# Kernel tuning notes

Hardware: AMD Instinct MI355X
Metric: run time of the kernel (lower is better)

## Reference

```python
import jax, jax.numpy as jnp
import numpy as np

EMBED = 768
HEADS = 12
HEAD_DIM = EMBED // HEADS
STREAMS = 4
SK_ITERS = 20
MLP_HIDDEN = 3072
EPS_SK = 1e-8
EPS_LN = 1e-5


def setup_inputs() -> dict:
    key = jax.random.key(0)
    ks = jax.random.split(key, 16)
    w = lambda k, shape: (jax.random.normal(k, shape, dtype=jnp.float32) * 0.02)
    return {
        "x": jax.random.normal(ks[0], (8, 1024, EMBED), dtype=jnp.float32),
        "ln1_g": jnp.ones((EMBED,), jnp.float32),
        "ln1_b": jnp.zeros((EMBED,), jnp.float32),
        "ln2_g": jnp.ones((EMBED,), jnp.float32),
        "ln2_b": jnp.zeros((EMBED,), jnp.float32),
        "qkv_w": w(ks[1], (3 * EMBED, EMBED)),
        "qkv_b": jnp.zeros((3 * EMBED,), jnp.float32),
        "proj_w": w(ks[2], (EMBED, EMBED)),
        "proj_b": jnp.zeros((EMBED,), jnp.float32),
        "fc1_w": w(ks[3], (MLP_HIDDEN, EMBED)),
        "fc1_b": jnp.zeros((MLP_HIDDEN,), jnp.float32),
        "fc2_w": w(ks[4], (EMBED, MLP_HIDDEN)),
        "fc2_b": jnp.zeros((EMBED,), jnp.float32),
        "a_hres": w(ks[5], (STREAMS, STREAMS)),
        "a_hpre": w(ks[6], (STREAMS,)),
        "a_hpost": w(ks[7], (STREAMS,)),
        "m_hres": w(ks[8], (STREAMS, STREAMS)),
        "m_hpre": w(ks[9], (STREAMS,)),
        "m_hpost": w(ks[10], (STREAMS,)),
    }


def layernorm(x, g, b):
    mu = x.mean(-1, keepdims=True)
    var = ((x - mu) ** 2).mean(-1, keepdims=True)
    return (x - mu) * jax.lax.rsqrt(var + EPS_LN) * g + b


def sinkhorn_knopp(logits):
    # logits: (n, n) -> doubly-stochastic (n, n); batch expansion in torch is redundant
    A = jnp.exp(logits)
    for _ in range(SK_ITERS):
        A = A / (A.sum(-1, keepdims=True) + EPS_SK)
        A = A / (A.sum(-2, keepdims=True) + EPS_SK)
    return A


def attention(x, qkv_w, qkv_b, proj_w, proj_b):
    B, N, D = x.shape
    qkv = x @ qkv_w.T + qkv_b                      # (B, N, 3D)
    qkv = qkv.reshape(B, N, 3, HEADS, HEAD_DIM)
    q, k, v = jnp.moveaxis(qkv, 2, 0)              # each (B, N, H, hd)
    scale = HEAD_DIM ** -0.5
    scores = jnp.einsum('bqhd,bkhd->bhqk', q, k) * scale
    attn = jax.nn.softmax(scores, axis=-1)
    out = jnp.einsum('bhqk,bkhd->bqhd', attn, v).reshape(B, N, D)
    return out @ proj_w.T + proj_b


def mlp(x, fc1_w, fc1_b, fc2_w, fc2_b):
    h = jax.nn.gelu(x @ fc1_w.T + fc1_b, approximate=False)
    return h @ fc2_w.T + fc2_b


def mhc(x, hres_logits, hpre_logits, hpost_logits, transform_fn):
    B, L, D = x.shape
    n, c = STREAMS, D // STREAMS
    xs = x.reshape(B, L, n, c)
    H_res = sinkhorn_knopp(hres_logits)            # (n, n)
    H_pre = jax.nn.softmax(hpre_logits)            # (n,)
    H_post = jax.nn.softmax(hpost_logits)          # (n,)
    x_pre = jnp.einsum('n,blnc->blc', H_pre, xs)   # weighted sum over streams
    x_pre_full = jnp.tile(x_pre, (1, 1, n))        # (B, L, D)
    t = transform_fn(x_pre_full)
    t_mean = t.reshape(B, L, n, c).mean(axis=2)    # (B, L, c)
    out = (jnp.einsum('nm,blmc->blnc', H_res, xs)
           + H_post[None, None, :, None] * t_mean[:, :, None, :])
    return out.reshape(B, L, D)


def reference(x, ln1_g, ln1_b, ln2_g, ln2_b, qkv_w, qkv_b, proj_w, proj_b,
              fc1_w, fc1_b, fc2_w, fc2_b,
              a_hres, a_hpre, a_hpost, m_hres, m_hpre, m_hpost):
    x = mhc(x, a_hres, a_hpre, a_hpost,
            lambda h: attention(layernorm(h, ln1_g, ln1_b), qkv_w, qkv_b, proj_w, proj_b))
    x = mhc(x, m_hres, m_hpre, m_hpost,
            lambda h: mlp(layernorm(h, ln2_g, ln2_b), fc1_w, fc1_b, fc2_w, fc2_b))
    return x
```

## Files before the change

kernel.cpp:

```cpp
#include <hip/hip_runtime.h>
#include <hip/hip_bf16.h>
#include <cstdint>
#include <cstddef>

#define EMBED 768
#define STREAMS 4
#define CHUNK 192
#define HEADS 12
#define HD 64
#define SEQ 1024
#define BATCH 8
#define TOKENS (BATCH * SEQ)
#define MLPH 3072

typedef __bf16 bf16;
typedef __bf16 bf16x4 __attribute__((ext_vector_type(4)));
typedef __bf16 bf16x8 __attribute__((ext_vector_type(8)));
typedef float f32x4 __attribute__((ext_vector_type(4)));
typedef float f32x16 __attribute__((ext_vector_type(16)));

#define GLDS16(gp, lp)                                                        \
  __builtin_amdgcn_global_load_lds(                                           \
      (const __attribute__((address_space(1))) void*)(gp),                    \
      (__attribute__((address_space(3))) void*)(lp), 16, 0, 0)

#define BARRIER() do { asm volatile("" ::: "memory");                         \
  __builtin_amdgcn_s_barrier(); asm volatile("" ::: "memory"); } while (0)

__global__ void hprep_kernel(const float* ar, const float* ap, const float* ao,
                             const float* mr, const float* mp, const float* mo,
                             float* HS) {
  if (threadIdx.x != 0) return;
  const float* L[2] = {ar, mr};
  const float* P[2] = {ap, mp};
  const float* O[2] = {ao, mo};
  for (int s = 0; s < 2; ++s) {
    float A[16];
    for (int i = 0; i < 16; ++i) A[i] = expf(L[s][i]);
    for (int it = 0; it < 20; ++it) {
      for (int r = 0; r < 4; ++r) {
        float rs = A[4*r] + A[4*r+1] + A[4*r+2] + A[4*r+3] + 1e-8f;
        for (int c = 0; c < 4; ++c) A[4*r+c] /= rs;
      }
      for (int c = 0; c < 4; ++c) {
        float cs = A[c] + A[4+c] + A[8+c] + A[12+c] + 1e-8f;
        for (int r = 0; r < 4; ++r) A[4*r+c] /= cs;
      }
    }
    float* dst = HS + s * 24;
    for (int i = 0; i < 16; ++i) dst[i] = A[i];
    {
      float m = fmaxf(fmaxf(P[s][0], P[s][1]), fmaxf(P[s][2], P[s][3]));
      float e[4], t = 0.f;
      for (int i = 0; i < 4; ++i) { e[i] = expf(P[s][i] - m); t += e[i]; }
      for (int i = 0; i < 4; ++i) dst[16 + i] = e[i] / t;
    }
    {
      float m = fmaxf(fmaxf(O[s][0], O[s][1]), fmaxf(O[s][2], O[s][3]));
      float e[4], t = 0.f;
      for (int i = 0; i < 4; ++i) { e[i] = expf(O[s][i] - m); t += e[i]; }
      for (int i = 0; i < 4; ++i) dst[20 + i] = e[i] / t;
    }
  }
}

__global__ void cvt_kernel(const float* __restrict__ in, bf16* __restrict__ out, int n4) {
  int i = blockIdx.x * 256 + threadIdx.x;
  const int st = gridDim.x * 256;
  for (; i < n4; i += st) {
    const float4 v = ((const float4*)in)[i];
    bf16x4 o = {(bf16)v.x, (bf16)v.y, (bf16)v.z, (bf16)v.w};
    *(bf16x4*)(out + (size_t)i * 4) = o;
  }
}

__global__ __launch_bounds__(256) void preln_kernel(
    const float* __restrict__ x, const float* __restrict__ H,
    const float* __restrict__ g, const float* __restrict__ b,
    bf16* __restrict__ out) {
  const int t = blockIdx.x;
  const float* xr = x + (size_t)t * EMBED;
  __shared__ float s[CHUNK];
  __shared__ float part[8];
  __shared__ float red[2];
  const int tid = threadIdx.x;
  float sv = 0.f;
  if (tid < CHUNK) {
    sv = H[0]*xr[tid] + H[1]*xr[CHUNK+tid] + H[2]*xr[2*CHUNK+tid] + H[3]*xr[3*CHUNK+tid];
    s[tid] = sv;
  }
  float sum = sv, sq = sv * sv;
  #pragma unroll
  for (int m = 32; m > 0; m >>= 1) {
    sum += __shfl_down(sum, m);
    sq  += __shfl_down(sq, m);
  }
  if ((tid & 63) == 0) { part[tid >> 6] = sum; part[4 + (tid >> 6)] = sq; }
  __syncthreads();
  if (tid == 0) {
    float S = part[0] + part[1] + part[2] + part[3];
    float Q = part[4] + part[5] + part[6] + part[7];
    float mu = S * (1.f / CHUNK);
    float var = Q * (1.f / CHUNK) - mu * mu;
    red[0] = mu;
    red[1] = rsqrtf(var + 1e-5f);
  }
  __syncthreads();
  const float mu = red[0], rs = red[1];
  bf16* orow = out + (size_t)t * EMBED;
  #pragma unroll
  for (int r = 0; r < 3; ++r) {
    const int d = tid + r * 256;
    const float v = (s[d % CHUNK] - mu) * rs * g[d] + b[d];
    orow[d] = (bf16)v;
  }
}

template <int GELU, int OUTF32>
__global__ __launch_bounds__(256) void gemm_bt(
    const bf16* __restrict__ A, const bf16* __restrict__ B,
    const float* __restrict__ bias, void* __restrict__ Cout,
    int M, int N, int K) {
  constexpr int BM = 128, BN = 128, BK = 32;
  __shared__ bf16 sA[3][BM * BK];
  __shared__ bf16 sB[3][BN * BK];
  const int tid  = threadIdx.x;
  const int lane = tid & 63;
  const int nwg = gridDim.x * gridDim.y;
  int Lw = blockIdx.y * gridDim.x + blockIdx.x;
  Lw = (Lw & 7) * (nwg >> 3) + (Lw >> 3);
  const int bm = (Lw / gridDim.x) * BM;
  const int bn = (Lw % gridDim.x) * BN;
  const int wave = tid >> 6;
  const int wr = (wave >> 1) * 64;
  const int wc = (wave & 1) * 64;
  f32x16 acc[2][2] = {};
  const int tr = tid >> 2;
  const int gt = tid & 3;
  const int gsw = (gt ^ ((tr >> 1) & 3)) * 8;
  const bf16* Ag = A + (size_t)(bm + tr) * K + gsw;
  const bf16* Bg = B + (size_t)(bn + tr) * K + gsw;
  const int lofs = tr * BK + gt * 8;
  const int r31 = lane & 31, rh = lane >> 5;
  const int asw = (r31 >> 1) & 3;
  const int nst = K / BK;
#define STAGE(buf, t)                                                         \
  do { const int bk_ = (t) * BK;                                              \
    GLDS16(Ag + bk_, sA[buf] + lofs);                                         \
    GLDS16(Ag + (size_t)64 * K + bk_, sA[buf] + lofs + 64 * BK);              \
    GLDS16(Bg + bk_, sB[buf] + lofs);                                         \
    GLDS16(Bg + (size_t)64 * K + bk_, sB[buf] + lofs + 64 * BK);              \
  } while (0)
  STAGE(0, 0);
  STAGE(1, 1);
  int cur = 0;
  for (int t = 0; t < nst; ++t) {
    if (t + 2 < nst) {
      const int nb = cur + 2 >= 3 ? cur - 1 : cur + 2;
      STAGE(nb, t + 2);
      asm volatile("s_waitcnt vmcnt(8)" ::: "memory");
    } else if (t + 1 < nst) {
      asm volatile("s_waitcnt vmcnt(4)" ::: "memory");
    } else {
      asm volatile("s_waitcnt vmcnt(0)" ::: "memory");
    }
    BARRIER();
    bf16x8 af[2][2], bfr[2][2];
    #pragma unroll
    for (int i = 0; i < 2; ++i)
      #pragma unroll
      for (int ks = 0; ks < 2; ++ks) {
        const int pos = ((ks * 2 + rh) ^ asw) * 8;
        af[i][ks]  = *(const bf16x8*)(sA[cur] + (wr + i * 32 + r31) * BK + pos);
        bfr[i][ks] = *(const bf16x8*)(sB[cur] + (wc + i * 32 + r31) * BK + pos);
      }
    #pragma unroll
    for (int ks = 0; ks < 2; ++ks)
      #pragma unroll
      for (int i = 0; i < 2; ++i)
        #pragma unroll
        for (int j = 0; j < 2; ++j)
          acc[i][j] = __builtin_amdgcn_mfma_f32_32x32x16_bf16(af[i][ks], bfr[j][ks], acc[i][j], 0, 0, 0);
    BARRIER();
    cur = cur == 2 ? 0 : cur + 1;
  }
#undef STAGE
  #pragma unroll
  for (int j = 0; j < 2; ++j) {
    const int col = bn + wc + j * 32 + r31;
    const float bv = bias[col];
    #pragma unroll
    for (int i = 0; i < 2; ++i) {
      const int row0 = bm + wr + i * 32 + 4 * rh;
      #pragma unroll
      for (int reg = 0; reg < 16; ++reg) {
        const int row = row0 + (reg & 3) + 8 * (reg >> 2);
        float v = acc[i][j][reg] + bv;
        if (GELU) v = 0.5f * v * (1.f + erff(v * 0.70710678118654752f));
        const size_t off = (size_t)row * N + col;
        if (OUTF32) ((float*)Cout)[off] = v;
        else        ((bf16*)Cout)[off] = (bf16)v;
      }
    }
  }
}

__global__ __launch_bounds__(256) void vt_kernel(const bf16* __restrict__ qkv,
                                                 bf16* __restrict__ VT) {
  const int tt = blockIdx.x;
  const int bh = blockIdx.y;
  const int bb = bh / HEADS;
  const int h = bh - bb * HEADS;
  __shared__ bf16 sT[64 * 64];
  const int t = threadIdx.x;
  const int srow = t >> 3;
  const int g = t & 7;
  const int gs = ((g ^ (srow & 7)) * 8);
  const bf16* Vg = qkv + ((size_t)(bb * SEQ + tt * 64 + srow)) * 2304 + 1536 + h * 64;
  GLDS16(Vg + gs, sT + srow * 64 + g * 8);
  GLDS16(Vg + (size_t)32 * 2304 + gs, sT + (32 + srow) * 64 + g * 8);
  __syncthreads();
  const int hd = t >> 2;
  const int tg = (t & 3) * 16;
  bf16 tmp[16];
  #pragma unroll
  for (int j = 0; j < 16; ++j) {
    const int tok = tg + j;
    tmp[j] = sT[tok * 64 + (hd ^ ((tok & 7) << 3))];
  }
  bf16* op = VT + (size_t)bh * (HD * SEQ) + (size_t)hd * SEQ + tt * 64 + tg;
  *(bf16x8*)(op) = *(const bf16x8*)(tmp);
  *(bf16x8*)(op + 8) = *(const bf16x8*)(tmp + 8);
}

__global__ __launch_bounds__(256) void attn_kernel(
    const bf16* __restrict__ qkv, const bf16* __restrict__ VT,
    bf16* __restrict__ out) {
  const int lin = blockIdx.x;
  const int qt = (lin >> 3) & 15;
  const int bh = (lin & 7) + 8 * (lin >> 7);
  const int bb = bh / HEADS;
  const int h = bh - bb * HEADS;
  const int tid = threadIdx.x;
  const int lane = tid & 63;
  const int wave = tid >> 6;
  const size_t tokBase = (size_t)bb * SEQ;
  const int q0 = qt * 64;

  __shared__ bf16 sQ[64 * 64];
  __shared__ bf16 sK[2][64 * 64];
  __shared__ bf16 sV[2][80 * 64];
  __shared__ bf16 sP[4][16 * 64];

  for (int idx = tid; idx < 16 * 64; idx += 256) {
    const bf16 v = (idx < 64) ? (bf16)1.f : (bf16)0.f;
    sV[0][64 * 64 + idx] = v;
    sV[1][64 * 64 + idx] = v;
  }

  const int srow = tid >> 3;
  const int g = tid & 7;
  const int gs = ((g ^ (srow & 7)) * 8);
  {
    const bf16* Qg = qkv + (tokBase + q0 + srow) * 2304 + h * 64;
    GLDS16(Qg + gs, sQ + srow * 64 + g * 8);
    GLDS16(Qg + (size_t)32 * 2304 + gs, sQ + (32 + srow) * 64 + g * 8);
  }
  __syncthreads();
  const int l15 = lane & 15, hi = lane >> 4;
  const int ksw = (l15 & 7) << 3;
  bf16x8 qf[2];
  {
    const int qrow = wave * 16 + l15;
    const int qsw = (qrow & 7) << 3;
    #pragma unroll
    for (int ks = 0; ks < 2; ++ks)
      qf[ks] = *(const bf16x8*)(sQ + qrow * 64 + ((hi * 8 + ks * 32) ^ qsw));
  }

  f32x4 o[5] = {};
  float mrun[4];
  #pragma unroll
  for (int r = 0; r < 4; ++r) mrun[r] = -1e30f;

  const bf16* Kbase = qkv + tokBase * 2304 + 768 + h * 64;
  const bf16* Vbase = VT + (size_t)bh * (HD * SEQ);

  {
    const bf16* Kg = Kbase + (size_t)srow * 2304;
    GLDS16(Kg + gs, sK[0] + srow * 64 + g * 8);
    GLDS16(Kg + (size_t)32 * 2304 + gs, sK[0] + (32 + srow) * 64 + g * 8);
    const bf16* Vg = Vbase + (size_t)srow * SEQ;
    GLDS16(Vg + gs, sV[0] + srow * 64 + g * 8);
    GLDS16(Vg + (size_t)32 * SEQ + gs, sV[0] + (32 + srow) * 64 + g * 8);
  }

  for (int it = 0; it < SEQ / 64; ++it) {
    const int cur = it & 1;
    if (it + 1 < SEQ / 64) {
      const int kb = (it + 1) * 64;
      const bf16* Kg = Kbase + (size_t)(kb + srow) * 2304;
      GLDS16(Kg + gs, sK[cur ^ 1] + srow * 64 + g * 8);
      GLDS16(Kg + (size_t)32 * 2304 + gs, sK[cur ^ 1] + (32 + srow) * 64 + g * 8);
      const bf16* Vg = Vbase + (size_t)srow * SEQ + kb;
      GLDS16(Vg + gs, sV[cur ^ 1] + srow * 64 + g * 8);
      GLDS16(Vg + (size_t)32 * SEQ + gs, sV[cur ^ 1] + (32 + srow) * 64 + g * 8);
      asm volatile("s_waitcnt vmcnt(4)" ::: "memory");
    } else {
      asm volatile("s_waitcnt vmcnt(0)" ::: "memory");
    }
    BARRIER();
    f32x4 s[4];
    #pragma unroll
    for (int nj = 0; nj < 4; ++nj) {
      s[nj] = (f32x4){0.f, 0.f, 0.f, 0.f};
      #pragma unroll
      for (int ks = 0; ks < 2; ++ks) {
        bf16x8 kf = *(const bf16x8*)(sK[cur] + (nj * 16 + l15) * 64 + ((hi * 8 + ks * 32) ^ ksw));
        s[nj] = __builtin_amdgcn_mfma_f32_16x16x32_bf16(qf[ks], kf, s[nj], 0, 0, 0);
      }
    }
    float tmax[4];
    #pragma unroll
    for (int r = 0; r < 4; ++r) {
      float m = fmaxf(fmaxf(s[0][r], s[1][r]), fmaxf(s[2][r], s[3][r]));
      tmax[r] = m * 0.125f;
    }
    #pragma unroll
    for (int r = 0; r < 4; ++r) {
      #pragma unroll
      for (int mm = 1; mm < 16; mm <<= 1) tmax[r] = fmaxf(tmax[r], __shfl_xor(tmax[r], mm));
    }
    bool need = false;
    #pragma unroll
    for (int r = 0; r < 4; ++r) need |= (tmax[r] > mrun[r]);
    if (__any(need)) {
      float alpha[4];
      #pragma unroll
      for (int r = 0; r < 4; ++r) {
        const float mnew = fmaxf(mrun[r], tmax[r]);
        alpha[r] = __expf(mrun[r] - mnew);
        mrun[r] = mnew;
      }
      #pragma unroll
      for (int nj = 0; nj < 5; ++nj)
        #pragma unroll
        for (int r = 0; r < 4; ++r)
          o[nj][r] *= alpha[r];
    }
    float p[4][4];
    #pragma unroll
    for (int r = 0; r < 4; ++r)
      #pragma unroll
      for (int nj = 0; nj < 4; ++nj)
        p[nj][r] = __expf(s[nj][r] * 0.125f - mrun[r]);
    bf16* Pw = sP[wave];
    #pragma unroll
    for (int r = 0; r < 4; ++r) {
      const int prow = hi * 4 + r;
      const int psw = (prow & 7) << 3;
      #pragma unroll
      for (int nj = 0; nj < 4; ++nj)
        Pw[prow * 64 + ((nj * 16 + l15) ^ psw)] = (bf16)p[nj][r];
    }
    #pragma unroll
    for (int ks = 0; ks < 2; ++ks) {
      bf16x8 pa = *(const bf16x8*)(Pw + l15 * 64 + ((hi * 8 + ks * 32) ^ ksw));
      #pragma unroll
      for (int nj = 0; nj < 5; ++nj) {
        bf16x8 vb = *(const bf16x8*)(sV[cur] + (nj * 16 + l15) * 64 + ((hi * 8 + ks * 32) ^ ksw));
        o[nj] = __builtin_amdgcn_mfma_f32_16x16x32_bf16(pa, vb, o[nj], 0, 0, 0);
      }
    }
    BARRIER();
  }
  #pragma unroll
  for (int r = 0; r < 4; ++r) {
    const float lsum = __shfl(o[4][r], hi << 4, 64);
    const float inv = 1.f / lsum;
    const size_t row = tokBase + q0 + wave * 16 + hi * 4 + r;
    bf16* orow = out + row * EMBED + h * 64;
    #pragma unroll
    for (int nj = 0; nj < 4; ++nj)
      orow[nj * 16 + l15] = (bf16)(o[nj][r] * inv);
  }
}

__global__ void combine_kernel(const float* __restrict__ xs, const float* __restrict__ t,
                               const float* __restrict__ Hres, const float* __restrict__ Hpost,
                               float* __restrict__ outp) {
  const int idx = blockIdx.x * 256 + threadIdx.x;
  if (idx >= TOKENS * CHUNK) return;
  const int tok = idx / CHUNK;
  const int c = idx - tok * CHUNK;
  const float* xr = xs + (size_t)tok * EMBED + c;
  const float* tr = t + (size_t)tok * EMBED + c;
  const float x0 = xr[0], x1 = xr[CHUNK], x2 = xr[2 * CHUNK], x3 = xr[3 * CHUNK];
  const float tm = 0.25f * (tr[0] + tr[CHUNK] + tr[2 * CHUNK] + tr[3 * CHUNK]);
  #pragma unroll
  for (int n = 0; n < 4; ++n) {
    const float v = Hres[4*n+0]*x0 + Hres[4*n+1]*x1 + Hres[4*n+2]*x2 + Hres[4*n+3]*x3
                  + Hpost[n] * tm;
    outp[(size_t)tok * EMBED + n * CHUNK + c] = v;
  }
}

extern "C" void kernel_launch(void* const* d_in, const int* in_sizes, int n_in,
                              void* d_out, int out_size, void* d_ws, size_t ws_size,
                              hipStream_t stream) {
  const float* x       = (const float*)d_in[0];
  const float* ln1_g   = (const float*)d_in[1];
  const float* ln1_b   = (const float*)d_in[2];
  const float* ln2_g   = (const float*)d_in[3];
  const float* ln2_b   = (const float*)d_in[4];
  const float* qkv_w   = (const float*)d_in[5];
  const float* qkv_b   = (const float*)d_in[6];
  const float* proj_w  = (const float*)d_in[7];
  const float* proj_b  = (const float*)d_in[8];
  const float* fc1_w   = (const float*)d_in[9];
  const float* fc1_b   = (const float*)d_in[10];
  const float* fc2_w   = (const float*)d_in[11];
  const float* fc2_b   = (const float*)d_in[12];
  const float* a_hres  = (const float*)d_in[13];
  const float* a_hpre  = (const float*)d_in[14];
  const float* a_hpost = (const float*)d_in[15];
  const float* m_hres  = (const float*)d_in[16];
  const float* m_hpre  = (const float*)d_in[17];
  const float* m_hpost = (const float*)d_in[18];

  char* ws = (char*)d_ws;
  float* HS = (float*)(ws);
  bf16* Wq  = (bf16*)(ws + 1024);
  bf16* Wp  = (bf16*)(ws + 1024 + 3538944);
  bf16* W1  = (bf16*)(ws + 1024 + 3538944 + 1179648);
  bf16* W2  = (bf16*)(ws + 1024 + 3538944 + 1179648 + 4718592);
  bf16* LN  = (bf16*)(ws + 14156800);
  float* T  = (float*)(ws + 26739712);
  float* X2 = (float*)(ws + 51905536);
  bf16* QKV = (bf16*)(ws + 77071360);
  bf16* AO  = (bf16*)(ws + 114820096);
  bf16* Hm  = (bf16*)(ws + 77071360);
  bf16* VT  = LN;

  hprep_kernel<<<1, 64, 0, stream>>>(a_hres, a_hpre, a_hpost, m_hres, m_hpre, m_hpost, HS);
  cvt_kernel<<<1024, 256, 0, stream>>>(qkv_w, Wq, 2304 * 768 / 4);
  cvt_kernel<<<1024, 256, 0, stream>>>(proj_w, Wp, 768 * 768 / 4);
  cvt_kernel<<<1024, 256, 0, stream>>>(fc1_w, W1, 3072 * 768 / 4);
  cvt_kernel<<<1024, 256, 0, stream>>>(fc2_w, W2, 768 * 3072 / 4);

  preln_kernel<<<TOKENS, 256, 0, stream>>>(x, HS + 16, ln1_g, ln1_b, LN);
  gemm_bt<0, 0><<<dim3(2304 / 128, TOKENS / 128), 256, 0, stream>>>(LN, Wq, qkv_b, QKV, TOKENS, 2304, 768);
  vt_kernel<<<dim3(16, 96), 256, 0, stream>>>(QKV, VT);
  attn_kernel<<<1536, 256, 0, stream>>>(QKV, VT, AO);
  gemm_bt<0, 1><<<dim3(768 / 128, TOKENS / 128), 256, 0, stream>>>(AO, Wp, proj_b, T, TOKENS, 768, 768);
  combine_kernel<<<(TOKENS * CHUNK + 255) / 256, 256, 0, stream>>>(x, T, HS + 0, HS + 20, X2);

  preln_kernel<<<TOKENS, 256, 0, stream>>>(X2, HS + 24 + 16, ln2_g, ln2_b, LN);
  gemm_bt<1, 0><<<dim3(3072 / 128, TOKENS / 128), 256, 0, stream>>>(LN, W1, fc1_b, Hm, TOKENS, 3072, 768);
  gemm_bt<0, 1><<<dim3(768 / 128, TOKENS / 128), 256, 0, stream>>>(Hm, W2, fc2_b, T, TOKENS, 768, 3072);
  combine_kernel<<<(TOKENS * CHUNK + 255) / 256, 256, 0, stream>>>(X2, T, HS + 24, HS + 24 + 20, (float*)d_out);
}
```

Measured before the change: 375.5 us.

## Widen GEMM N-tile to 256 and split-K the fc2 GEMM with partial sum in combine

The GEMM kernel is templated on its N tile width, and the QKV and fc1 GEMMs now use 256-wide tiles for more reuse of the A operand per block. The fc2 GEMM (K=3072, only 384 blocks) is split along K into two halves that write separate fp32 partials, and the combine kernel adds the second partial, raising parallelism to fill more CUs. Launch bounds now request two waves per SIMD. The trade-offs are a larger accumulator footprint with register pressure risk, plus extra fp32 partial traffic. Split-K only runs if the workspace is large enough.

```diff
diff --git a/kernel.cpp b/kernel.cpp
--- a/kernel.cpp
+++ b/kernel.cpp
@@ -116,12 +116,14 @@
   }
 }
 
-template <int GELU, int OUTF32>
-__global__ __launch_bounds__(256) void gemm_bt(
+template <int BN, int GELU, int OUTF32, int KSPLIT>
+__global__ __launch_bounds__(256, 2) void gemm_bt(
     const bf16* __restrict__ A, const bf16* __restrict__ B,
-    const float* __restrict__ bias, void* __restrict__ Cout,
-    int M, int N, int K) {
-  constexpr int BM = 128, BN = 128, BK = 32;
+    const float* __restrict__ bias, void* __restrict__ C0,
+    void* __restrict__ C1, int M, int N, int K) {
+  constexpr int BM = 128, BK = 32;
+  constexpr int NJ = BN / 64;
+  constexpr int BLD = BN / 64;
   __shared__ bf16 sA[3][BM * BK];
   __shared__ bf16 sB[3][BN * BK];
   const int tid  = threadIdx.x;
@@ -133,23 +135,25 @@
   const int bn = (Lw % gridDim.x) * BN;
   const int wave = tid >> 6;
   const int wr = (wave >> 1) * 64;
-  const int wc = (wave & 1) * 64;
-  f32x16 acc[2][2] = {};
+  const int wc = (wave & 1) * (BN / 2);
+  f32x16 acc[2][NJ] = {};
   const int tr = tid >> 2;
   const int gt = tid & 3;
   const int gsw = (gt ^ ((tr >> 1) & 3)) * 8;
-  const bf16* Ag = A + (size_t)(bm + tr) * K + gsw;
-  const bf16* Bg = B + (size_t)(bn + tr) * K + gsw;
+  const int kbeg = (KSPLIT > 1) ? blockIdx.z * (K / KSPLIT) : 0;
+  const bf16* Ag = A + (size_t)(bm + tr) * K + kbeg + gsw;
+  const bf16* Bg = B + (size_t)(bn + tr) * K + kbeg + gsw;
   const int lofs = tr * BK + gt * 8;
   const int r31 = lane & 31, rh = lane >> 5;
   const int asw = (r31 >> 1) & 3;
-  const int nst = K / BK;
+  const int nst = K / KSPLIT / BK;
 #define STAGE(buf, t)                                                         \
   do { const int bk_ = (t) * BK;                                              \
     GLDS16(Ag + bk_, sA[buf] + lofs);                                         \
     GLDS16(Ag + (size_t)64 * K + bk_, sA[buf] + lofs + 64 * BK);              \
-    GLDS16(Bg + bk_, sB[buf] + lofs);                                         \
-    GLDS16(Bg + (size_t)64 * K + bk_, sB[buf] + lofs + 64 * BK);              \
+    _Pragma("unroll")                                                         \
+    for (int u = 0; u < BLD; ++u)                                             \
+      GLDS16(Bg + (size_t)(u * 64) * K + bk_, sB[buf] + lofs + u * 64 * BK);  \
   } while (0)
   STAGE(0, 0);
   STAGE(1, 1);
@@ -158,37 +162,43 @@
     if (t + 2 < nst) {
       const int nb = cur + 2 >= 3 ? cur - 1 : cur + 2;
       STAGE(nb, t + 2);
-      asm volatile("s_waitcnt vmcnt(8)" ::: "memory");
+      if constexpr (BN == 128) asm volatile("s_waitcnt vmcnt(8)" ::: "memory");
+      else                     asm volatile("s_waitcnt vmcnt(12)" ::: "memory");
     } else if (t + 1 < nst) {
-      asm volatile("s_waitcnt vmcnt(4)" ::: "memory");
+      if constexpr (BN == 128) asm volatile("s_waitcnt vmcnt(4)" ::: "memory");
+      else                     asm volatile("s_waitcnt vmcnt(6)" ::: "memory");
     } else {
       asm volatile("s_waitcnt vmcnt(0)" ::: "memory");
     }
     BARRIER();
-    bf16x8 af[2][2], bfr[2][2];
-    #pragma unroll
-    for (int i = 0; i < 2; ++i)
-      #pragma unroll
-      for (int ks = 0; ks < 2; ++ks) {
-        const int pos = ((ks * 2 + rh) ^ asw) * 8;
-        af[i][ks]  = *(const bf16x8*)(sA[cur] + (wr + i * 32 + r31) * BK + pos);
-        bfr[i][ks] = *(const bf16x8*)(sB[cur] + (wc + i * 32 + r31) * BK + pos);
-      }
+    bf16x8 af[2][2], bfr[NJ][2];
+    #pragma unroll
+    for (int ks = 0; ks < 2; ++ks) {
+      const int pos = ((ks * 2 + rh) ^ asw) * 8;
+      #pragma unroll
+      for (int i = 0; i < 2; ++i)
+        af[i][ks] = *(const bf16x8*)(sA[cur] + (wr + i * 32 + r31) * BK + pos);
+      #pragma unroll
+      for (int j = 0; j < NJ; ++j)
+        bfr[j][ks] = *(const bf16x8*)(sB[cur] + (wc + j * 32 + r31) * BK + pos);
+    }
     #pragma unroll
     for (int ks = 0; ks < 2; ++ks)
       #pragma unroll
       for (int i = 0; i < 2; ++i)
         #pragma unroll
-        for (int j = 0; j < 2; ++j)
+        for (int j = 0; j < NJ; ++j)
           acc[i][j] = __builtin_amdgcn_mfma_f32_32x32x16_bf16(af[i][ks], bfr[j][ks], acc[i][j], 0, 0, 0);
     BARRIER();
     cur = cur == 2 ? 0 : cur + 1;
   }
 #undef STAGE
-  #pragma unroll
-  for (int j = 0; j < 2; ++j) {
+  const bool second = (KSPLIT > 1) && (blockIdx.z != 0);
+  void* Co = second ? C1 : C0;
+  #pragma unroll
+  for (int j = 0; j < NJ; ++j) {
     const int col = bn + wc + j * 32 + r31;
-    const float bv = bias[col];
+    const float bv = second ? 0.f : bias[col];
     #pragma unroll
     for (int i = 0; i < 2; ++i) {
       const int row0 = bm + wr + i * 32 + 4 * rh;
@@ -198,8 +208,8 @@
         float v = acc[i][j][reg] + bv;
         if (GELU) v = 0.5f * v * (1.f + erff(v * 0.70710678118654752f));
         const size_t off = (size_t)row * N + col;
-        if (OUTF32) ((float*)Cout)[off] = v;
-        else        ((bf16*)Cout)[off] = (bf16)v;
+        if (OUTF32) ((float*)Co)[off] = v;
+        else        ((bf16*)Co)[off] = (bf16)v;
       }
     }
   }
@@ -386,7 +396,9 @@
   }
 }
 
+template <int TWO>
 __global__ void combine_kernel(const float* __restrict__ xs, const float* __restrict__ t,
+                               const float* __restrict__ t2,
                                const float* __restrict__ Hres, const float* __restrict__ Hpost,
                                float* __restrict__ outp) {
   const int idx = blockIdx.x * 256 + threadIdx.x;
@@ -396,7 +408,12 @@
   const float* xr = xs + (size_t)tok * EMBED + c;
   const float* tr = t + (size_t)tok * EMBED + c;
   const float x0 = xr[0], x1 = xr[CHUNK], x2 = xr[2 * CHUNK], x3 = xr[3 * CHUNK];
-  const float tm = 0.25f * (tr[0] + tr[CHUNK] + tr[2 * CHUNK] + tr[3 * CHUNK]);
+  float tm = tr[0] + tr[CHUNK] + tr[2 * CHUNK] + tr[3 * CHUNK];
+  if (TWO) {
+    const float* t2r = t2 + (size_t)tok * EMBED + c;
+    tm += t2r[0] + t2r[CHUNK] + t2r[2 * CHUNK] + t2r[3 * CHUNK];
+  }
+  tm *= 0.25f;
   #pragma unroll
   for (int n = 0; n < 4; ++n) {
     const float v = Hres[4*n+0]*x0 + Hres[4*n+1]*x1 + Hres[4*n+2]*x2 + Hres[4*n+3]*x3
@@ -441,6 +458,8 @@
   bf16* AO  = (bf16*)(ws + 114820096);
   bf16* Hm  = (bf16*)(ws + 77071360);
   bf16* VT  = LN;
+  float* PT = (float*)(ws + 127403008);
+  const bool haveP = ws_size >= (size_t)127403008 + (size_t)TOKENS * EMBED * 4;
 
   hprep_kernel<<<1, 64, 0, stream>>>(a_hres, a_hpre, a_hpost, m_hres, m_hpre, m_hpost, HS);
   cvt_kernel<<<1024, 256, 0, stream>>>(qkv_w, Wq, 2304 * 768 / 4);
@@ -449,14 +468,27 @@
   cvt_kernel<<<1024, 256, 0, stream>>>(fc2_w, W2, 768 * 3072 / 4);
 
   preln_kernel<<<TOKENS, 256, 0, stream>>>(x, HS + 16, ln1_g, ln1_b, LN);
-  gemm_bt<0, 0><<<dim3(2304 / 128, TOKENS / 128), 256, 0, stream>>>(LN, Wq, qkv_b, QKV, TOKENS, 2304, 768);
+  gemm_bt<256, 0, 0, 1><<<dim3(2304 / 256, TOKENS / 128), 256, 0, stream>>>(
+      LN, Wq, qkv_b, QKV, nullptr, TOKENS, 2304, 768);
   vt_kernel<<<dim3(16, 96), 256, 0, stream>>>(QKV, VT);
   attn_kernel<<<1536, 256, 0, stream>>>(QKV, VT, AO);
-  gemm_bt<0, 1><<<dim3(768 / 128, TOKENS / 128), 256, 0, stream>>>(AO, Wp, proj_b, T, TOKENS, 768, 768);
-  combine_kernel<<<(TOKENS * CHUNK + 255) / 256, 256, 0, stream>>>(x, T, HS + 0, HS + 20, X2);
+  gemm_bt<128, 0, 1, 1><<<dim3(768 / 128, TOKENS / 128), 256, 0, stream>>>(
+      AO, Wp, proj_b, T, nullptr, TOKENS, 768, 768);
+  combine_kernel<0><<<(TOKENS * CHUNK + 255) / 256, 256, 0, stream>>>(
+      x, T, nullptr, HS + 0, HS + 20, X2);
 
   preln_kernel<<<TOKENS, 256, 0, stream>>>(X2, HS + 24 + 16, ln2_g, ln2_b, LN);
-  gemm_bt<1, 0><<<dim3(3072 / 128, TOKENS / 128), 256, 0, stream>>>(LN, W1, fc1_b, Hm, TOKENS, 3072, 768);
-  gemm_bt<0, 1><<<dim3(768 / 128, TOKENS / 128), 256, 0, stream>>>(Hm, W2, fc2_b, T, TOKENS, 768, 3072);
-  combine_kernel<<<(TOKENS * CHUNK + 255) / 256, 256, 0, stream>>>(X2, T, HS + 24, HS + 24 + 20, (float*)d_out);
-}
+  gemm_bt<256, 1, 0, 1><<<dim3(3072 / 256, TOKENS / 128), 256, 0, stream>>>(
+      LN, W1, fc1_b, Hm, nullptr, TOKENS, 3072, 768);
+  if (haveP) {
+    gemm_bt<128, 0, 1, 2><<<dim3(768 / 128, TOKENS / 128, 2), 256, 0, stream>>>(
+        Hm, W2, fc2_b, T, PT, TOKENS, 768, 3072);
+    combine_kernel<1><<<(TOKENS * CHUNK + 255) / 256, 256, 0, stream>>>(
+        X2, T, PT, HS + 24, HS + 24 + 20, (float*)d_out);
+  } else {
+    gemm_bt<128, 0, 1, 1><<<dim3(768 / 128, TOKENS / 128), 256, 0, stream>>>(
+        Hm, W2, fc2_b, T, nullptr, TOKENS, 768, 3072);
+    combine_kernel<0><<<(TOKENS * CHUNK + 255) / 256, 256, 0, stream>>>(
+        X2, T, nullptr, HS + 24, HS + 24 + 20, (float*)d_out);
+  }
+}
```

After: 378.8 us. Within noise of the previous version (+0.9%).
